# Performance work log

Hardware: AMD Instinct MI355X
Metric: run time of the kernel (lower is better)

The kernel has to match this reference:

```python
import jax, jax.numpy as jnp
import numpy as np
import math

H, DK, G_DIM, S_DIM, HID = 8, 64, 512, 3072, 512
B = 16384
EPS = 1e-5

def _layernorm(x, g, b):
    mu = jnp.mean(x, axis=-1, keepdims=True)
    var = jnp.mean((x - mu) ** 2, axis=-1, keepdims=True)
    return (x - mu) * jax.lax.rsqrt(var + EPS) * g + b

def setup_inputs() -> dict:
    key = jax.random.key(0)
    ks = jax.random.split(key, 12)
    s = 0.02
    return {
        "h_g": jax.random.normal(ks[0], (B, G_DIM), jnp.float32),
        "h_s": jax.random.normal(ks[1], (B, S_DIM), jnp.float32),
        # stacked per-head projections: [H, in_dim, d_k]
        "Wq": jax.random.normal(ks[2], (H, G_DIM, DK), jnp.float32) * s,
        "bq": jnp.zeros((H, DK), jnp.float32),
        "Wk": jax.random.normal(ks[3], (H, S_DIM, DK), jnp.float32) * s,
        "bk": jnp.zeros((H, DK), jnp.float32),
        "Wv": jax.random.normal(ks[4], (H, S_DIM, DK), jnp.float32) * s,
        "bv": jnp.zeros((H, DK), jnp.float32),
        "Wo": jax.random.normal(ks[5], (HID, HID), jnp.float32) * s,
        "bo": jnp.zeros((HID,), jnp.float32),
        "ln1_g": jnp.ones((HID,), jnp.float32),
        "ln1_b": jnp.zeros((HID,), jnp.float32),
        "W1": jax.random.normal(ks[6], (HID, 2 * HID), jnp.float32) * s,
        "b1": jnp.zeros((2 * HID,), jnp.float32),
        "W2": jax.random.normal(ks[7], (2 * HID, HID), jnp.float32) * s,
        "b2": jnp.zeros((HID,), jnp.float32),
        "ln2_g": jnp.ones((HID,), jnp.float32),
        "ln2_b": jnp.zeros((HID,), jnp.float32),
    }

def reference(h_g, h_s, Wq, bq, Wk, bk, Wv, bv, Wo, bo, ln1_g, ln1_b, W1, b1, W2, b2, ln2_g, ln2_b):
    b = h_g.shape[0]
    # batched per-head projections (fuses the per-head Linear loop)
    Q = jnp.einsum('bg,hgd->bhd', h_g, Wq) + bq          # [B,H,DK]
    K = jnp.einsum('bs,hsd->bhd', h_s, Wk) + bk          # [B,H,DK]
    V = jnp.einsum('bs,hsd->bhd', h_s, Wv) + bv          # [B,H,DK]
    # seq_len == 1: scores is [B,H,1]; softmax over a single key == 1
    scores = jnp.sum(Q * K, axis=-1, keepdims=True) / math.sqrt(DK)
    attn_w = jax.nn.softmax(scores, axis=-1)             # identically ones
    attn = attn_w * V                                    # == V
    h_concat = attn.reshape(b, H * DK)                   # [B,HID]
    h_attn = h_concat @ Wo + bo
    h_attn = _layernorm(h_attn + h_g, ln1_g, ln1_b)
    # MLP (dropout is identity in eval mode); torch GELU default = exact erf
    h = jax.nn.gelu(h_attn @ W1 + b1, approximate=False) @ W2 + b2
    return _layernorm(h + h_attn, ln2_g, ln2_b)
```

## Files before the change

kernel.cpp:

```cpp
#include <hip/hip_runtime.h>
#include <hip/hip_bf16.h>
#include <math.h>

#define HH    8
#define DKK   64
#define GD    512
#define SD    3072
#define HID_  512
#define BB    16384

typedef unsigned short ushort_t;
typedef __attribute__((ext_vector_type(8))) short bf16x8;
typedef __attribute__((ext_vector_type(4))) float f32x4;

__device__ __forceinline__ float bf2f(ushort_t u) {
  union { unsigned int i; float f; } c; c.i = ((unsigned int)u) << 16; return c.f;
}
__device__ __forceinline__ ushort_t f2bf(float f) {
  union { float f; unsigned int i; } c; c.f = f;
  unsigned int x = c.i;
  return (ushort_t)((x + 0x7FFFu + ((x >> 16) & 1u)) >> 16);
}
__device__ __forceinline__ unsigned int pk_bf16(float a, float b) {
  __hip_bfloat162 h = __float22bfloat162_rn(make_float2(a, b));
  union { __hip_bfloat162 h; unsigned int u; } c; c.h = h; return c.u;
}

__device__ __forceinline__ void async_cp16(const ushort_t* gsrc, ushort_t* ldst) {
  __builtin_amdgcn_global_load_lds(
      (const __attribute__((address_space(1))) unsigned int*)gsrc,
      (__attribute__((address_space(3))) unsigned int*)ldst, 16, 0, 0);
}
__device__ __forceinline__ void async_cp16f(const float* gsrc, float* ldst) {
  __builtin_amdgcn_global_load_lds(
      (const __attribute__((address_space(1))) unsigned int*)gsrc,
      (__attribute__((address_space(3))) unsigned int*)ldst, 16, 0, 0);
}

__device__ __forceinline__ float gelu_tanh(float x) {
  float y = 0.79788456080286535588f * (x + 0.044715f * x * x * x);
  float e = __expf(2.0f * y);
  float th = 1.0f - 2.0f / (e + 1.0f);
  return 0.5f * x * (1.0f + th);
}

__device__ __forceinline__ void swz_coords(int& nb, int& mb, int& kz) {
  int NB = gridDim.x, MB = gridDim.y;
  int bid = blockIdx.x + NB * (blockIdx.y + MB * blockIdx.z);
  int xcd = bid & 7;
  int j = bid >> 3;
  nb = j & (NB - 1);
  int rest = j / NB;
  int mk = (rest << 3) | xcd;
  mb = mk & (MB - 1);
  kz = mk / MB;
}

template <int EPI, int SWZ>
__global__ __launch_bounds__(256) void gemm_bt(
    const ushort_t* __restrict__ A, const ushort_t* __restrict__ Bt,
    void* __restrict__ Cv, const float* __restrict__ bias,
    int M, int N, int Kfull, int Klen) {
  __shared__ __align__(16) ushort_t As[128 * 32];
  __shared__ __align__(16) ushort_t Bs[128 * 32];
  const int tid = threadIdx.x;
  const int wv = tid >> 6;
  const int lane = tid & 63;
  int nb, mb, kz;
  if (SWZ) swz_coords(nb, mb, kz);
  else { nb = blockIdx.x; mb = blockIdx.y; kz = blockIdx.z; }
  const int m0 = mb * 128, n0 = nb * 128, kbeg = kz * Klen;
  const int srow = lane >> 2;
  const int scol = (lane & 3) * 8;
  const int wm = wv & 1, wn = wv >> 1;
  const int lr = lane & 15, quad = lane >> 4;

  f32x4 acc[4][4];
#pragma unroll
  for (int i = 0; i < 4; ++i)
#pragma unroll
    for (int j = 0; j < 4; ++j) acc[i][j] = (f32x4){0.f, 0.f, 0.f, 0.f};

  const ushort_t* Ab = A + (size_t)m0 * Kfull + kbeg;
  const ushort_t* Bb = Bt + (size_t)n0 * Kfull + kbeg;

  for (int k0 = 0; k0 < Klen; k0 += 32) {
    __syncthreads();
#pragma unroll
    for (int i = 0; i < 2; ++i) {
      const int chunk = i * 4 + wv;
      const int row = chunk * 16 + srow;
      async_cp16(Ab + (size_t)row * Kfull + (k0 + scol), As + chunk * 512);
      async_cp16(Bb + (size_t)row * Kfull + (k0 + scol), Bs + chunk * 512);
    }
    __syncthreads();
    bf16x8 af[4], bfr[4];
#pragma unroll
    for (int i = 0; i < 4; ++i)
      af[i] = *(const bf16x8*)&As[(wm * 64 + i * 16 + lr) * 32 + quad * 8];
#pragma unroll
    for (int j = 0; j < 4; ++j)
      bfr[j] = *(const bf16x8*)&Bs[(wn * 64 + j * 16 + lr) * 32 + quad * 8];
#pragma unroll
    for (int i = 0; i < 4; ++i)
#pragma unroll
      for (int j = 0; j < 4; ++j)
        acc[i][j] = __builtin_amdgcn_mfma_f32_16x16x32_bf16(af[i], bfr[j], acc[i][j], 0, 0, 0);
  }

#pragma unroll
  for (int i = 0; i < 4; ++i) {
    const int mg = m0 + wm * 64 + i * 16 + quad * 4;
#pragma unroll
    for (int j = 0; j < 4; ++j) {
      const int ng = n0 + wn * 64 + j * 16 + lr;
      if (EPI == 2) {
        float* C = (float*)Cv + (size_t)kz * M * N;
#pragma unroll
        for (int r = 0; r < 4; ++r)
          C[(size_t)(mg + r) * N + ng] = acc[i][j][r];
      } else {
        ushort_t* C = (ushort_t*)Cv;
        const float bvv = bias ? bias[ng] : 0.0f;
#pragma unroll
        for (int r = 0; r < 4; ++r) {
          float v = acc[i][j][r] + bvv;
          if (EPI == 1) v = gelu_tanh(v);
          C[(size_t)(mg + r) * N + ng] = f2bf(v);
        }
      }
    }
  }
}

__global__ __launch_bounds__(256, 4) void gemm_a32(
    const float* __restrict__ A, const ushort_t* __restrict__ Bt,
    float* __restrict__ C, int M, int N, int Kfull, int Klen) {
  __shared__ __align__(16) float As4[128 * 32];
  __shared__ __align__(16) ushort_t Bs[128 * 32];
  const int tid = threadIdx.x;
  const int wv = tid >> 6;
  const int lane = tid & 63;
  int nb, mb, kz;
  swz_coords(nb, mb, kz);
  const int m0 = mb * 128, n0 = nb * 128, kbeg = kz * Klen;
  const int srow = lane >> 2;
  const int scol = (lane & 3) * 8;
  const int wm = wv & 1, wn = wv >> 1;
  const int lr = lane & 15, quad = lane >> 4;
  const int a_rc = lane >> 3;
  const int a_g = (lane & 7) ^ a_rc;

  f32x4 acc[4][4];
#pragma unroll
  for (int i = 0; i < 4; ++i)
#pragma unroll
    for (int j = 0; j < 4; ++j) acc[i][j] = (f32x4){0.f, 0.f, 0.f, 0.f};

  const float* Ab = A + (size_t)m0 * Kfull + kbeg;
  const ushort_t* Bb = Bt + (size_t)n0 * Kfull + kbeg;

  for (int k0 = 0; k0 < Klen; k0 += 32) {
    __syncthreads();
#pragma unroll
    for (int i = 0; i < 2; ++i) {
      const int chunk = i * 4 + wv;
      const int row = chunk * 16 + srow;
      async_cp16(Bb + (size_t)row * Kfull + (k0 + scol), Bs + chunk * 512);
    }
#pragma unroll
    for (int t = 0; t < 4; ++t) {
      const int chunkA = t * 4 + wv;
      const int r = chunkA * 8 + a_rc;
      async_cp16f(Ab + (size_t)r * Kfull + (k0 + 4 * a_g), As4 + chunkA * 256);
    }
    __syncthreads();
    bf16x8 af[4], bfr[4];
#pragma unroll
    for (int i = 0; i < 4; ++i) {
      const int r = wm * 64 + i * 16 + lr;
      const int x0 = (2 * quad) ^ (lr & 7);
      const int x1 = (2 * quad + 1) ^ (lr & 7);
      float4 fa = *(const float4*)&As4[r * 32 + x0 * 4];
      float4 fb = *(const float4*)&As4[r * 32 + x1 * 4];
      union { unsigned int u[4]; bf16x8 v; } c;
      c.u[0] = pk_bf16(fa.x, fa.y); c.u[1] = pk_bf16(fa.z, fa.w);
      c.u[2] = pk_bf16(fb.x, fb.y); c.u[3] = pk_bf16(fb.z, fb.w);
      af[i] = c.v;
    }
#pragma unroll
    for (int j = 0; j < 4; ++j)
      bfr[j] = *(const bf16x8*)&Bs[(wn * 64 + j * 16 + lr) * 32 + quad * 8];
#pragma unroll
    for (int i = 0; i < 4; ++i)
#pragma unroll
      for (int j = 0; j < 4; ++j)
        acc[i][j] = __builtin_amdgcn_mfma_f32_16x16x32_bf16(af[i], bfr[j], acc[i][j], 0, 0, 0);
  }

  float* Cp = C + (size_t)kz * M * N;
#pragma unroll
  for (int i = 0; i < 4; ++i) {
    const int mg = m0 + wm * 64 + i * 16 + quad * 4;
#pragma unroll
    for (int j = 0; j < 4; ++j) {
      const int ng = n0 + wn * 64 + j * 16 + lr;
#pragma unroll
      for (int r = 0; r < 4; ++r)
        Cp[(size_t)(mg + r) * N + ng] = acc[i][j][r];
    }
  }
}

__global__ __launch_bounds__(256) void permute_wv(const float* __restrict__ Wv,
                                                  ushort_t* __restrict__ Wvp) {
  const int idx = (blockIdx.x * 256 + threadIdx.x) * 8;
  const int s = idx >> 9;
  const int c = idx & 511;
  const float* src = Wv + (size_t)(c >> 6) * (SD * DKK) + (size_t)s * DKK + (c & 63);
  float4 a = *(const float4*)src;
  float4 b = *(const float4*)(src + 4);
  unsigned int p[4];
  p[0] = pk_bf16(a.x, a.y); p[1] = pk_bf16(a.z, a.w);
  p[2] = pk_bf16(b.x, b.y); p[3] = pk_bf16(b.z, b.w);
  *(uint4*)(Wvp + idx) = *(const uint4*)p;
}

__global__ __launch_bounds__(256) void transpose3(
    const float* __restrict__ s0, ushort_t* __restrict__ d0,
    const float* __restrict__ s1, ushort_t* __restrict__ d1,
    const float* __restrict__ s2, ushort_t* __restrict__ d2) {
  __shared__ ushort_t tile[32][33];
  const int z = blockIdx.z;
  const float* src = (z == 0) ? s0 : (z == 1) ? s1 : s2;
  ushort_t* dst = (z == 0) ? d0 : (z == 1) ? d1 : d2;
  const int R = (z == 2) ? 1024 : 512;
  const int C = (z == 1) ? 1024 : 512;
  const int bx = blockIdx.x * 32;
  const int by = blockIdx.y * 32;
  if (bx >= C || by >= R) return;
  const int tx = threadIdx.x, ty = threadIdx.y;
#pragma unroll
  for (int i = 0; i < 32; i += 8)
    tile[ty + i][tx] = f2bf(src[(size_t)(by + ty + i) * C + (bx + tx)]);
  __syncthreads();
#pragma unroll
  for (int i = 0; i < 32; i += 8)
    dst[(size_t)(bx + ty + i) * R + (by + tx)] = tile[tx][ty + i];
}

__global__ __launch_bounds__(256) void c0_kernel(const float* __restrict__ bv,
                                                 const float* __restrict__ Wo,
                                                 const float* __restrict__ bo,
                                                 float* __restrict__ c0) {
  __shared__ float red[8][32];
  const int jl = threadIdx.x & 31;
  const int chunk = threadIdx.x >> 5;
  const int j = blockIdx.x * 32 + jl;
  const int cbase = chunk * 64;
  float s = 0.f;
#pragma unroll 8
  for (int c = 0; c < 64; ++c) s += bv[cbase + c] * Wo[(size_t)(cbase + c) * 512 + j];
  red[chunk][jl] = s;
  __syncthreads();
  if (chunk == 0) {
    float t = bo[j];
#pragma unroll
    for (int q = 0; q < 8; ++q) t += red[q][jl];
    c0[j] = t;
  }
}

template <int RES_F32, int OUT_F32>
__global__ __launch_bounds__(256) void ln_fused(const float* __restrict__ p0,
                                                const float* __restrict__ p1,
                                                const float* __restrict__ cb,
                                                const void* __restrict__ res_,
                                                const float* __restrict__ g,
                                                const float* __restrict__ b,
                                                void* __restrict__ out_) {
  const int row = blockIdx.x * 4 + (threadIdx.x >> 6);
  const int lane = threadIdx.x & 63;
  const size_t base = (size_t)row * 512 + lane * 8;
  const int col = lane * 8;
  float4 a0 = *(const float4*)(p0 + base);
  float4 a1 = *(const float4*)(p0 + base + 4);
  float4 c0v = *(const float4*)(p1 + base);
  float4 c1v = *(const float4*)(p1 + base + 4);
  float4 d0 = *(const float4*)(cb + col);
  float4 d1 = *(const float4*)(cb + col + 4);
  float t[8];
  t[0] = a0.x + c0v.x + d0.x; t[1] = a0.y + c0v.y + d0.y;
  t[2] = a0.z + c0v.z + d0.z; t[3] = a0.w + c0v.w + d0.w;
  t[4] = a1.x + c1v.x + d1.x; t[5] = a1.y + c1v.y + d1.y;
  t[6] = a1.z + c1v.z + d1.z; t[7] = a1.w + c1v.w + d1.w;
  float r[8];
  if (RES_F32) {
    const float* res = (const float*)res_;
    float4 e0 = *(const float4*)(res + base);
    float4 e1 = *(const float4*)(res + base + 4);
    r[0] = e0.x; r[1] = e0.y; r[2] = e0.z; r[3] = e0.w;
    r[4] = e1.x; r[5] = e1.y; r[6] = e1.z; r[7] = e1.w;
  } else {
    const ushort_t* res = (const ushort_t*)res_;
    uint4 rv = *(const uint4*)(res + base);
    const ushort_t* rp = (const ushort_t*)&rv;
#pragma unroll
    for (int k = 0; k < 8; ++k) r[k] = bf2f(rp[k]);
  }
  float x[8];
  float s = 0.f, sq = 0.f;
#pragma unroll
  for (int k = 0; k < 8; ++k) {
    float v = t[k] + r[k];
    x[k] = v; s += v; sq += v * v;
  }
#pragma unroll
  for (int off = 32; off > 0; off >>= 1) {
    s += __shfl_xor(s, off);
    sq += __shfl_xor(sq, off);
  }
  const float mean = s * (1.0f / 512.0f);
  const float var = sq * (1.0f / 512.0f) - mean * mean;
  const float rstd = rsqrtf(var + 1e-5f);
  float4 gv0 = *(const float4*)(g + col);
  float4 gv1 = *(const float4*)(g + col + 4);
  float4 bv0 = *(const float4*)(b + col);
  float4 bv1 = *(const float4*)(b + col + 4);
  const float gg[8] = {gv0.x, gv0.y, gv0.z, gv0.w, gv1.x, gv1.y, gv1.z, gv1.w};
  const float bb[8] = {bv0.x, bv0.y, bv0.z, bv0.w, bv1.x, bv1.y, bv1.z, bv1.w};
  float y[8];
#pragma unroll
  for (int k = 0; k < 8; ++k) y[k] = (x[k] - mean) * rstd * gg[k] + bb[k];
  if (OUT_F32) {
    float* out = (float*)out_;
    *(float4*)(out + base) = make_float4(y[0], y[1], y[2], y[3]);
    *(float4*)(out + base + 4) = make_float4(y[4], y[5], y[6], y[7]);
  } else {
    ushort_t* out = (ushort_t*)out_;
    uint4 ov; ushort_t* op = (ushort_t*)&ov;
#pragma unroll
    for (int k = 0; k < 8; ++k) op[k] = f2bf(y[k]);
    *(uint4*)(out + base) = ov;
  }
}

extern "C" void kernel_launch(void* const* d_in, const int* in_sizes, int n_in,
                              void* d_out, int out_size, void* d_ws, size_t ws_size,
                              hipStream_t stream) {
  const float* h_g  = (const float*)d_in[0];
  const float* h_s  = (const float*)d_in[1];
  const float* Wv   = (const float*)d_in[6];
  const float* bv   = (const float*)d_in[7];
  const float* Wo   = (const float*)d_in[8];
  const float* bo   = (const float*)d_in[9];
  const float* ln1g = (const float*)d_in[10];
  const float* ln1b = (const float*)d_in[11];
  const float* W1   = (const float*)d_in[12];
  const float* b1   = (const float*)d_in[13];
  const float* W2   = (const float*)d_in[14];
  const float* b2   = (const float*)d_in[15];
  const float* ln2g = (const float*)d_in[16];
  const float* ln2b = (const float*)d_in[17];

  char* ws = (char*)d_ws;
  ushort_t* WoT = (ushort_t*)(ws + 0);
  ushort_t* W1T = (ushort_t*)(ws + 524288);
  ushort_t* W2T = (ushort_t*)(ws + 1572864);
  ushort_t* Wvp = (ushort_t*)(ws + 2621440);
  ushort_t* WcT = (ushort_t*)(ws + 5767168);
  float*    c0f = (float*)(ws + 8912896);
  float*    p0  = (float*)(ws + 16777216);
  float*    p1  = (float*)(ws + 50331648);
  ushort_t* x   = (ushort_t*)(ws + 83886080);
  ushort_t* u   = (ushort_t*)(ws + 100663296);
  float*    q0  = p0;
  float*    q1  = p1;
  (void)in_sizes; (void)n_in; (void)out_size; (void)ws_size;

  hipLaunchKernelGGL(permute_wv, dim3(768), dim3(256), 0, stream, Wv, Wvp);
  hipLaunchKernelGGL(transpose3, dim3(32, 32, 3), dim3(32, 8), 0, stream,
                     Wo, WoT, W1, W1T, W2, W2T);
  hipLaunchKernelGGL(c0_kernel, dim3(16), dim3(256), 0, stream, bv, Wo, bo, c0f);

  hipLaunchKernelGGL((gemm_bt<0, 0>), dim3(24, 4, 1), dim3(256), 0, stream,
                     WoT, Wvp, (void*)WcT, (const float*)nullptr, 512, 3072, 512, 512);
  hipLaunchKernelGGL(gemm_a32, dim3(4, 128, 2), dim3(256), 0, stream,
                     h_s, WcT, p0, BB, 512, 3072, 1536);
  hipLaunchKernelGGL((ln_fused<1, 0>), dim3(4096), dim3(256), 0, stream,
                     p0, p1, c0f, (const void*)h_g, ln1g, ln1b, (void*)x);
  hipLaunchKernelGGL((gemm_bt<1, 1>), dim3(8, 128, 1), dim3(256), 0, stream,
                     x, W1T, (void*)u, b1, BB, 1024, 512, 512);
  hipLaunchKernelGGL((gemm_bt<2, 1>), dim3(4, 128, 2), dim3(256), 0, stream,
                     u, W2T, (void*)q0, (const float*)nullptr, BB, 512, 1024, 512);
  hipLaunchKernelGGL((ln_fused<0, 1>), dim3(4096), dim3(256), 0, stream,
                     q0, q1, b2, (const void*)x, ln2g, ln2b, d_out);
}
```

Baseline: 548.6 us.

## Double-buffer LDS tiles in both GEMM kernels to overlap loads with MFMA

Both GEMM kernels now keep two shared-memory buffers per operand. The next K-tile's async global-to-LDS copies are issued right after the barrier, so they run while the current tile feeds the MFMAs. This also cuts the main loop to one barrier per tile, hiding global-memory latency that was previously exposed on each iteration. In exchange, LDS per block doubles, which for gemm_a32 (48KB) may lower the number of resident blocks per CU below its launch bound.

```diff
diff --git a/kernel.cpp b/kernel.cpp
--- a/kernel.cpp
+++ b/kernel.cpp
@@ -61,8 +61,8 @@
     const ushort_t* __restrict__ A, const ushort_t* __restrict__ Bt,
     void* __restrict__ Cv, const float* __restrict__ bias,
     int M, int N, int Kfull, int Klen) {
-  __shared__ __align__(16) ushort_t As[128 * 32];
-  __shared__ __align__(16) ushort_t Bs[128 * 32];
+  __shared__ __align__(16) ushort_t As[2][128 * 32];
+  __shared__ __align__(16) ushort_t Bs[2][128 * 32];
   const int tid = threadIdx.x;
   const int wv = tid >> 6;
   const int lane = tid & 63;
@@ -84,23 +84,29 @@
   const ushort_t* Ab = A + (size_t)m0 * Kfull + kbeg;
   const ushort_t* Bb = Bt + (size_t)n0 * Kfull + kbeg;
 
-  for (int k0 = 0; k0 < Klen; k0 += 32) {
-    __syncthreads();
+  auto stage = [&](int k0, int b) {
 #pragma unroll
     for (int i = 0; i < 2; ++i) {
       const int chunk = i * 4 + wv;
       const int row = chunk * 16 + srow;
-      async_cp16(Ab + (size_t)row * Kfull + (k0 + scol), As + chunk * 512);
-      async_cp16(Bb + (size_t)row * Kfull + (k0 + scol), Bs + chunk * 512);
-    }
+      async_cp16(Ab + (size_t)row * Kfull + (k0 + scol), &As[b][chunk * 512]);
+      async_cp16(Bb + (size_t)row * Kfull + (k0 + scol), &Bs[b][chunk * 512]);
+    }
+  };
+
+  const int nt = Klen >> 5;
+  stage(0, 0);
+  int buf = 0;
+  for (int t = 0; t < nt; ++t, buf ^= 1) {
     __syncthreads();
+    if (t + 1 < nt) stage((t + 1) << 5, buf ^ 1);
     bf16x8 af[4], bfr[4];
 #pragma unroll
     for (int i = 0; i < 4; ++i)
-      af[i] = *(const bf16x8*)&As[(wm * 64 + i * 16 + lr) * 32 + quad * 8];
+      af[i] = *(const bf16x8*)&As[buf][(wm * 64 + i * 16 + lr) * 32 + quad * 8];
 #pragma unroll
     for (int j = 0; j < 4; ++j)
-      bfr[j] = *(const bf16x8*)&Bs[(wn * 64 + j * 16 + lr) * 32 + quad * 8];
+      bfr[j] = *(const bf16x8*)&Bs[buf][(wn * 64 + j * 16 + lr) * 32 + quad * 8];
 #pragma unroll
     for (int i = 0; i < 4; ++i)
 #pragma unroll
@@ -136,8 +142,8 @@
 __global__ __launch_bounds__(256, 4) void gemm_a32(
     const float* __restrict__ A, const ushort_t* __restrict__ Bt,
     float* __restrict__ C, int M, int N, int Kfull, int Klen) {
-  __shared__ __align__(16) float As4[128 * 32];
-  __shared__ __align__(16) ushort_t Bs[128 * 32];
+  __shared__ __align__(16) float As4[2][128 * 32];
+  __shared__ __align__(16) ushort_t Bs[2][128 * 32];
   const int tid = threadIdx.x;
   const int wv = tid >> 6;
   const int lane = tid & 63;
@@ -160,29 +166,35 @@
   const float* Ab = A + (size_t)m0 * Kfull + kbeg;
   const ushort_t* Bb = Bt + (size_t)n0 * Kfull + kbeg;
 
-  for (int k0 = 0; k0 < Klen; k0 += 32) {
-    __syncthreads();
+  auto stage = [&](int k0, int b) {
 #pragma unroll
     for (int i = 0; i < 2; ++i) {
       const int chunk = i * 4 + wv;
       const int row = chunk * 16 + srow;
-      async_cp16(Bb + (size_t)row * Kfull + (k0 + scol), Bs + chunk * 512);
-    }
-#pragma unroll
-    for (int t = 0; t < 4; ++t) {
-      const int chunkA = t * 4 + wv;
+      async_cp16(Bb + (size_t)row * Kfull + (k0 + scol), &Bs[b][chunk * 512]);
+    }
+#pragma unroll
+    for (int t4 = 0; t4 < 4; ++t4) {
+      const int chunkA = t4 * 4 + wv;
       const int r = chunkA * 8 + a_rc;
-      async_cp16f(Ab + (size_t)r * Kfull + (k0 + 4 * a_g), As4 + chunkA * 256);
-    }
+      async_cp16f(Ab + (size_t)r * Kfull + (k0 + 4 * a_g), &As4[b][chunkA * 256]);
+    }
+  };
+
+  const int nt = Klen >> 5;
+  stage(0, 0);
+  int buf = 0;
+  for (int t = 0; t < nt; ++t, buf ^= 1) {
     __syncthreads();
+    if (t + 1 < nt) stage((t + 1) << 5, buf ^ 1);
     bf16x8 af[4], bfr[4];
 #pragma unroll
     for (int i = 0; i < 4; ++i) {
       const int r = wm * 64 + i * 16 + lr;
       const int x0 = (2 * quad) ^ (lr & 7);
       const int x1 = (2 * quad + 1) ^ (lr & 7);
-      float4 fa = *(const float4*)&As4[r * 32 + x0 * 4];
-      float4 fb = *(const float4*)&As4[r * 32 + x1 * 4];
+      float4 fa = *(const float4*)&As4[buf][r * 32 + x0 * 4];
+      float4 fb = *(const float4*)&As4[buf][r * 32 + x1 * 4];
       union { unsigned int u[4]; bf16x8 v; } c;
       c.u[0] = pk_bf16(fa.x, fa.y); c.u[1] = pk_bf16(fa.z, fa.w);
       c.u[2] = pk_bf16(fb.x, fb.y); c.u[3] = pk_bf16(fb.z, fb.w);
@@ -190,7 +202,7 @@
     }
 #pragma unroll
     for (int j = 0; j < 4; ++j)
-      bfr[j] = *(const bf16x8*)&Bs[(wn * 64 + j * 16 + lr) * 32 + quad * 8];
+      bfr[j] = *(const bf16x8*)&Bs[buf][(wn * 64 + j * 16 + lr) * 32 + quad * 8];
 #pragma unroll
     for (int i = 0; i < 4; ++i)
 #pragma unroll
```

After: 549.4 us. No clear change (+0.1%).

## Double-buffer and swizzle LDS in GEMMs, shrink N tile to 64

Applied to the files above, without the earlier changes.

The bf16 GEMM kernel now double-buffers its LDS tiles, issuing the next K-slice copy before computing the current one, which needs only one barrier per iteration. Both GEMM kernels XOR-swizzle the LDS column slot to cut bank conflicts. They also move to a 64-wide N tile with higher occupancy hints and twice as many blocks. The intent is to overlap loads with MFMA work and raise occupancy. The cost is less reuse of the A tile per block, so A is re-read from global memory more often.

```diff
diff --git a/kernel.cpp b/kernel.cpp
--- a/kernel.cpp
+++ b/kernel.cpp
@@ -56,55 +56,68 @@
   kz = mk / MB;
 }
 
-template <int EPI, int SWZ>
-__global__ __launch_bounds__(256) void gemm_bt(
+template <int EPI, int SWZ, int BN>
+__global__ __launch_bounds__(256, (BN == 64) ? 6 : 2) void gemm_bt(
     const ushort_t* __restrict__ A, const ushort_t* __restrict__ Bt,
     void* __restrict__ Cv, const float* __restrict__ bias,
     int M, int N, int Kfull, int Klen) {
-  __shared__ __align__(16) ushort_t As[128 * 32];
-  __shared__ __align__(16) ushort_t Bs[128 * 32];
+  constexpr int NF = BN / 32;
+  __shared__ __align__(16) ushort_t As[2][128 * 32];
+  __shared__ __align__(16) ushort_t Bs[2][BN * 32];
   const int tid = threadIdx.x;
   const int wv = tid >> 6;
   const int lane = tid & 63;
   int nb, mb, kz;
   if (SWZ) swz_coords(nb, mb, kz);
   else { nb = blockIdx.x; mb = blockIdx.y; kz = blockIdx.z; }
-  const int m0 = mb * 128, n0 = nb * 128, kbeg = kz * Klen;
+  const int m0 = mb * 128, n0 = nb * BN, kbeg = kz * Klen;
   const int srow = lane >> 2;
-  const int scol = (lane & 3) * 8;
+  const int scolg = (((lane & 3) ^ ((lane >> 3) & 3))) * 8;
   const int wm = wv & 1, wn = wv >> 1;
   const int lr = lane & 15, quad = lane >> 4;
-
-  f32x4 acc[4][4];
+  const int slotx = (quad ^ ((lr >> 1) & 3)) * 8;
+
+  f32x4 acc[4][NF];
 #pragma unroll
   for (int i = 0; i < 4; ++i)
 #pragma unroll
-    for (int j = 0; j < 4; ++j) acc[i][j] = (f32x4){0.f, 0.f, 0.f, 0.f};
+    for (int j = 0; j < NF; ++j) acc[i][j] = (f32x4){0.f, 0.f, 0.f, 0.f};
 
   const ushort_t* Ab = A + (size_t)m0 * Kfull + kbeg;
   const ushort_t* Bb = Bt + (size_t)n0 * Kfull + kbeg;
 
-  for (int k0 = 0; k0 < Klen; k0 += 32) {
-    __syncthreads();
+  auto stage = [&](int k0, int b) {
 #pragma unroll
     for (int i = 0; i < 2; ++i) {
       const int chunk = i * 4 + wv;
       const int row = chunk * 16 + srow;
-      async_cp16(Ab + (size_t)row * Kfull + (k0 + scol), As + chunk * 512);
-      async_cp16(Bb + (size_t)row * Kfull + (k0 + scol), Bs + chunk * 512);
-    }
+      async_cp16(Ab + (size_t)row * Kfull + (k0 + scolg), &As[b][chunk * 512]);
+    }
+#pragma unroll
+    for (int i = 0; i < BN / 64; ++i) {
+      const int chunk = i * 4 + wv;
+      const int row = chunk * 16 + srow;
+      async_cp16(Bb + (size_t)row * Kfull + (k0 + scolg), &Bs[b][chunk * 512]);
+    }
+  };
+
+  const int nt = Klen >> 5;
+  stage(0, 0);
+  int buf = 0;
+  for (int t = 0; t < nt; ++t, buf ^= 1) {
     __syncthreads();
-    bf16x8 af[4], bfr[4];
+    if (t + 1 < nt) stage((t + 1) << 5, buf ^ 1);
+    bf16x8 af[4], bfr[NF];
 #pragma unroll
     for (int i = 0; i < 4; ++i)
-      af[i] = *(const bf16x8*)&As[(wm * 64 + i * 16 + lr) * 32 + quad * 8];
-#pragma unroll
-    for (int j = 0; j < 4; ++j)
-      bfr[j] = *(const bf16x8*)&Bs[(wn * 64 + j * 16 + lr) * 32 + quad * 8];
+      af[i] = *(const bf16x8*)&As[buf][(wm * 64 + i * 16 + lr) * 32 + slotx];
+#pragma unroll
+    for (int j = 0; j < NF; ++j)
+      bfr[j] = *(const bf16x8*)&Bs[buf][(wn * (NF * 16) + j * 16 + lr) * 32 + slotx];
 #pragma unroll
     for (int i = 0; i < 4; ++i)
 #pragma unroll
-      for (int j = 0; j < 4; ++j)
+      for (int j = 0; j < NF; ++j)
         acc[i][j] = __builtin_amdgcn_mfma_f32_16x16x32_bf16(af[i], bfr[j], acc[i][j], 0, 0, 0);
   }
 
@@ -112,8 +125,8 @@
   for (int i = 0; i < 4; ++i) {
     const int mg = m0 + wm * 64 + i * 16 + quad * 4;
 #pragma unroll
-    for (int j = 0; j < 4; ++j) {
-      const int ng = n0 + wn * 64 + j * 16 + lr;
+    for (int j = 0; j < NF; ++j) {
+      const int ng = n0 + wn * (NF * 16) + j * 16 + lr;
       if (EPI == 2) {
         float* C = (float*)Cv + (size_t)kz * M * N;
 #pragma unroll
@@ -133,49 +146,46 @@
   }
 }
 
-__global__ __launch_bounds__(256, 4) void gemm_a32(
+__global__ __launch_bounds__(256, 5) void gemm_a32(
     const float* __restrict__ A, const ushort_t* __restrict__ Bt,
     float* __restrict__ C, int M, int N, int Kfull, int Klen) {
   __shared__ __align__(16) float As4[128 * 32];
-  __shared__ __align__(16) ushort_t Bs[128 * 32];
+  __shared__ __align__(16) ushort_t Bs[64 * 32];
   const int tid = threadIdx.x;
   const int wv = tid >> 6;
   const int lane = tid & 63;
   int nb, mb, kz;
   swz_coords(nb, mb, kz);
-  const int m0 = mb * 128, n0 = nb * 128, kbeg = kz * Klen;
+  const int m0 = mb * 128, n0 = nb * 64, kbeg = kz * Klen;
   const int srow = lane >> 2;
-  const int scol = (lane & 3) * 8;
+  const int b_colg = (((lane & 3) ^ ((lane >> 3) & 3))) * 8;
   const int wm = wv & 1, wn = wv >> 1;
   const int lr = lane & 15, quad = lane >> 4;
+  const int slotx = (quad ^ ((lr >> 1) & 3)) * 8;
   const int a_rc = lane >> 3;
   const int a_g = (lane & 7) ^ a_rc;
 
-  f32x4 acc[4][4];
+  f32x4 acc[4][2];
 #pragma unroll
   for (int i = 0; i < 4; ++i)
 #pragma unroll
-    for (int j = 0; j < 4; ++j) acc[i][j] = (f32x4){0.f, 0.f, 0.f, 0.f};
+    for (int j = 0; j < 2; ++j) acc[i][j] = (f32x4){0.f, 0.f, 0.f, 0.f};
 
   const float* Ab = A + (size_t)m0 * Kfull + kbeg;
   const ushort_t* Bb = Bt + (size_t)n0 * Kfull + kbeg;
 
   for (int k0 = 0; k0 < Klen; k0 += 32) {
     __syncthreads();
-#pragma unroll
-    for (int i = 0; i < 2; ++i) {
-      const int chunk = i * 4 + wv;
-      const int row = chunk * 16 + srow;
-      async_cp16(Bb + (size_t)row * Kfull + (k0 + scol), Bs + chunk * 512);
-    }
-#pragma unroll
-    for (int t = 0; t < 4; ++t) {
-      const int chunkA = t * 4 + wv;
+    async_cp16(Bb + (size_t)(wv * 16 + srow) * Kfull + (k0 + b_colg),
+               Bs + wv * 512);
+#pragma unroll
+    for (int t4 = 0; t4 < 4; ++t4) {
+      const int chunkA = t4 * 4 + wv;
       const int r = chunkA * 8 + a_rc;
       async_cp16f(Ab + (size_t)r * Kfull + (k0 + 4 * a_g), As4 + chunkA * 256);
     }
     __syncthreads();
-    bf16x8 af[4], bfr[4];
+    bf16x8 af[4], bfr[2];
 #pragma unroll
     for (int i = 0; i < 4; ++i) {
       const int r = wm * 64 + i * 16 + lr;
@@ -189,12 +199,12 @@
       af[i] = c.v;
     }
 #pragma unroll
-    for (int j = 0; j < 4; ++j)
-      bfr[j] = *(const bf16x8*)&Bs[(wn * 64 + j * 16 + lr) * 32 + quad * 8];
+    for (int j = 0; j < 2; ++j)
+      bfr[j] = *(const bf16x8*)&Bs[(wn * 32 + j * 16 + lr) * 32 + slotx];
 #pragma unroll
     for (int i = 0; i < 4; ++i)
 #pragma unroll
-      for (int j = 0; j < 4; ++j)
+      for (int j = 0; j < 2; ++j)
         acc[i][j] = __builtin_amdgcn_mfma_f32_16x16x32_bf16(af[i], bfr[j], acc[i][j], 0, 0, 0);
   }
 
@@ -203,8 +213,8 @@
   for (int i = 0; i < 4; ++i) {
     const int mg = m0 + wm * 64 + i * 16 + quad * 4;
 #pragma unroll
-    for (int j = 0; j < 4; ++j) {
-      const int ng = n0 + wn * 64 + j * 16 + lr;
+    for (int j = 0; j < 2; ++j) {
+      const int ng = n0 + wn * 32 + j * 16 + lr;
 #pragma unroll
       for (int r = 0; r < 4; ++r)
         Cp[(size_t)(mg + r) * N + ng] = acc[i][j][r];
@@ -383,15 +393,15 @@
                      Wo, WoT, W1, W1T, W2, W2T);
   hipLaunchKernelGGL(c0_kernel, dim3(16), dim3(256), 0, stream, bv, Wo, bo, c0f);
 
-  hipLaunchKernelGGL((gemm_bt<0, 0>), dim3(24, 4, 1), dim3(256), 0, stream,
+  hipLaunchKernelGGL((gemm_bt<0, 0, 128>), dim3(24, 4, 1), dim3(256), 0, stream,
                      WoT, Wvp, (void*)WcT, (const float*)nullptr, 512, 3072, 512, 512);
-  hipLaunchKernelGGL(gemm_a32, dim3(4, 128, 2), dim3(256), 0, stream,
+  hipLaunchKernelGGL(gemm_a32, dim3(8, 128, 2), dim3(256), 0, stream,
                      h_s, WcT, p0, BB, 512, 3072, 1536);
   hipLaunchKernelGGL((ln_fused<1, 0>), dim3(4096), dim3(256), 0, stream,
                      p0, p1, c0f, (const void*)h_g, ln1g, ln1b, (void*)x);
-  hipLaunchKernelGGL((gemm_bt<1, 1>), dim3(8, 128, 1), dim3(256), 0, stream,
+  hipLaunchKernelGGL((gemm_bt<1, 1, 64>), dim3(16, 128, 1), dim3(256), 0, stream,
                      x, W1T, (void*)u, b1, BB, 1024, 512, 512);
-  hipLaunchKernelGGL((gemm_bt<2, 1>), dim3(4, 128, 2), dim3(256), 0, stream,
+  hipLaunchKernelGGL((gemm_bt<2, 1, 64>), dim3(8, 128, 2), dim3(256), 0, stream,
                      u, W2T, (void*)q0, (const float*)nullptr, BB, 512, 1024, 512);
   hipLaunchKernelGGL((ln_fused<0, 1>), dim3(4096), dim3(256), 0, stream,
                      q0, q1, b2, (const void*)x, ln2g, ln2b, d_out);
```

Result: slower. 578.4 us (+5.4%).

## Replace split-K fp32-A GEMM with 8-wave 128x256 double-buffered pipelined kernel

Applied to the files above, without the earlier changes.

The big h_s × WcT GEMM (K=3072) used a 128x128 tile, split-K over 2, and synchronous single-buffer staging. It now uses a 512-thread block computing a 128x256 tile over the full K. Tiles of 64 K-steps are double-buffered in 128KB of dynamic LDS, with async copies interleaved between MFMA phases, setprio, and XCD-aware block mapping. This removes the split-K partial buffer and lets the first LayerNorm read a single partial. The risk is lower occupancy and only 256 blocks, which may underfill the GPU.

```diff
diff --git a/kernel.cpp b/kernel.cpp
--- a/kernel.cpp
+++ b/kernel.cpp
@@ -133,23 +133,30 @@
   }
 }
 
-__global__ __launch_bounds__(256, 4) void gemm_a32(
+__global__ __launch_bounds__(512, 2) void gemm8_a32(
     const float* __restrict__ A, const ushort_t* __restrict__ Bt,
-    float* __restrict__ C, int M, int N, int Kfull, int Klen) {
-  __shared__ __align__(16) float As4[128 * 32];
-  __shared__ __align__(16) ushort_t Bs[128 * 32];
+    float* __restrict__ C, int M, int N, int K) {
+  extern __shared__ char smem[];
+  float* Af = (float*)smem;
+  ushort_t* Bsm = (ushort_t*)(smem + 65536);
   const int tid = threadIdx.x;
   const int wv = tid >> 6;
   const int lane = tid & 63;
-  int nb, mb, kz;
-  swz_coords(nb, mb, kz);
-  const int m0 = mb * 128, n0 = nb * 128, kbeg = kz * Klen;
-  const int srow = lane >> 2;
-  const int scol = (lane & 3) * 8;
-  const int wm = wv & 1, wn = wv >> 1;
   const int lr = lane & 15, quad = lane >> 4;
-  const int a_rc = lane >> 3;
-  const int a_g = (lane & 7) ^ a_rc;
+  const int wm = wv >> 2, wn = wv & 3;
+  const int bid = blockIdx.x + (int)gridDim.x * blockIdx.y;
+  const int xcd = bid & 7;
+  const int jj = bid >> 3;
+  const int nb = jj & 1;
+  const int mb = xcd * 16 + (jj >> 1);
+  const int m0 = mb * 128, n0 = nb * 256;
+
+  const int a_r0 = wv * 4 + (lane >> 4);
+  const int a_g = (lane & 15) ^ ((wv & 1) * 4 + (lane >> 4));
+  const float* Asrc = A + (size_t)(m0 + a_r0) * K + a_g * 4;
+  const int b_r0 = wv * 8 + (lane >> 3);
+  const int b_g = (lane & 7) ^ (lane >> 3);
+  const ushort_t* Bsrc = Bt + (size_t)(n0 + b_r0) * K + b_g * 8;
 
   f32x4 acc[4][4];
 #pragma unroll
@@ -157,57 +164,158 @@
 #pragma unroll
     for (int j = 0; j < 4; ++j) acc[i][j] = (f32x4){0.f, 0.f, 0.f, 0.f};
 
-  const float* Ab = A + (size_t)m0 * Kfull + kbeg;
-  const ushort_t* Bb = Bt + (size_t)n0 * Kfull + kbeg;
-
-  for (int k0 = 0; k0 < Klen; k0 += 32) {
-    __syncthreads();
+  auto stageA2 = [&](int k0, int b, int i0) {
 #pragma unroll
     for (int i = 0; i < 2; ++i) {
-      const int chunk = i * 4 + wv;
-      const int row = chunk * 16 + srow;
-      async_cp16(Bb + (size_t)row * Kfull + (k0 + scol), Bs + chunk * 512);
-    }
-#pragma unroll
-    for (int t = 0; t < 4; ++t) {
-      const int chunkA = t * 4 + wv;
-      const int r = chunkA * 8 + a_rc;
-      async_cp16f(Ab + (size_t)r * Kfull + (k0 + 4 * a_g), As4 + chunkA * 256);
-    }
-    __syncthreads();
-    bf16x8 af[4], bfr[4];
-#pragma unroll
-    for (int i = 0; i < 4; ++i) {
-      const int r = wm * 64 + i * 16 + lr;
-      const int x0 = (2 * quad) ^ (lr & 7);
-      const int x1 = (2 * quad + 1) ^ (lr & 7);
-      float4 fa = *(const float4*)&As4[r * 32 + x0 * 4];
-      float4 fb = *(const float4*)&As4[r * 32 + x1 * 4];
-      union { unsigned int u[4]; bf16x8 v; } c;
-      c.u[0] = pk_bf16(fa.x, fa.y); c.u[1] = pk_bf16(fa.z, fa.w);
-      c.u[2] = pk_bf16(fb.x, fb.y); c.u[3] = pk_bf16(fb.z, fb.w);
-      af[i] = c.v;
-    }
-#pragma unroll
-    for (int j = 0; j < 4; ++j)
-      bfr[j] = *(const bf16x8*)&Bs[(wn * 64 + j * 16 + lr) * 32 + quad * 8];
-#pragma unroll
-    for (int i = 0; i < 4; ++i)
-#pragma unroll
-      for (int j = 0; j < 4; ++j)
-        acc[i][j] = __builtin_amdgcn_mfma_f32_16x16x32_bf16(af[i], bfr[j], acc[i][j], 0, 0, 0);
-  }
-
-  float* Cp = C + (size_t)kz * M * N;
-#pragma unroll
-  for (int i = 0; i < 4; ++i) {
-    const int mg = m0 + wm * 64 + i * 16 + quad * 4;
-#pragma unroll
-    for (int j = 0; j < 4; ++j) {
-      const int ng = n0 + wn * 64 + j * 16 + lr;
+      const int ii = i0 + i;
+      async_cp16f(Asrc + (size_t)(ii * 32) * K + k0,
+                  Af + b * 8192 + ii * 2048 + wv * 256);
+    }
+  };
+  auto stageB2 = [&](int k0, int b, int i0) {
+#pragma unroll
+    for (int i = 0; i < 2; ++i) {
+      const int ii = i0 + i;
+      async_cp16(Bsrc + (size_t)(ii * 64) * K + k0,
+                 Bsm + b * 16384 + ii * 4096 + wv * 512);
+    }
+  };
+
+  stageA2(0, 0, 0); stageA2(0, 0, 2);
+  stageB2(0, 0, 0); stageB2(0, 0, 2);
+  stageA2(64, 1, 0); stageA2(64, 1, 2);
+  asm volatile("s_waitcnt vmcnt(4)" ::: "memory");
+  __builtin_amdgcn_sched_barrier(0);
+  __builtin_amdgcn_s_barrier();
+
+  const int nt = K >> 6;
+  for (int t = 0; t < nt; ++t) {
+    const int b = t & 1;
+    const int kB = (t + 1) << 6;
+    const int kA = (t + 2) << 6;
+    const bool hasB = (t + 1 < nt);
+    const bool hasA = (t + 2 < nt);
+    const float* Ab = Af + b * 8192;
+    const ushort_t* Bb = Bsm + b * 16384;
+
+    bf16x8 bfr[4][2];
+#pragma unroll
+    for (int jf = 0; jf < 4; ++jf) {
+      const int r = wn * 64 + jf * 16 + lr;
+#pragma unroll
+      for (int kk = 0; kk < 2; ++kk) {
+        const int pg = (kk * 4 + quad) ^ (lr & 7);
+        bfr[jf][kk] = *(const bf16x8*)(Bb + r * 64 + pg * 8);
+      }
+    }
+    bf16x8 af0[2], af1[2], af2[2], af3[2];
+    {
+      const float* base0 = Ab + (wm * 64 + 0 * 16 + lr) * 64;
+      const float* base1 = Ab + (wm * 64 + 1 * 16 + lr) * 64;
+#pragma unroll
+      for (int kk = 0; kk < 2; ++kk) {
+        const int g0 = (kk * 8 + 2 * quad) ^ (lr & 7);
+        const int g1 = (kk * 8 + 2 * quad + 1) ^ (lr & 7);
+        float4 fa = *(const float4*)(base0 + g0 * 4);
+        float4 fb = *(const float4*)(base0 + g1 * 4);
+        union { unsigned int u[4]; bf16x8 v; } c0;
+        c0.u[0] = pk_bf16(fa.x, fa.y); c0.u[1] = pk_bf16(fa.z, fa.w);
+        c0.u[2] = pk_bf16(fb.x, fb.y); c0.u[3] = pk_bf16(fb.z, fb.w);
+        af0[kk] = c0.v;
+        float4 ga = *(const float4*)(base1 + g0 * 4);
+        float4 gb = *(const float4*)(base1 + g1 * 4);
+        union { unsigned int u[4]; bf16x8 v; } c1;
+        c1.u[0] = pk_bf16(ga.x, ga.y); c1.u[1] = pk_bf16(ga.z, ga.w);
+        c1.u[2] = pk_bf16(gb.x, gb.y); c1.u[3] = pk_bf16(gb.z, gb.w);
+        af1[kk] = c1.v;
+      }
+    }
+    if (hasB) stageB2(kB, b ^ 1, 0);
+    __builtin_amdgcn_s_barrier();
+    __builtin_amdgcn_s_setprio(1);
+#pragma unroll
+    for (int jf = 0; jf < 4; ++jf) {
+      acc[0][jf] = __builtin_amdgcn_mfma_f32_16x16x32_bf16(af0[0], bfr[jf][0], acc[0][jf], 0, 0, 0);
+      acc[0][jf] = __builtin_amdgcn_mfma_f32_16x16x32_bf16(af0[1], bfr[jf][1], acc[0][jf], 0, 0, 0);
+    }
+    __builtin_amdgcn_s_setprio(0);
+    asm volatile("s_waitcnt lgkmcnt(0)" ::: "memory");
+    __builtin_amdgcn_sched_barrier(0);
+    __builtin_amdgcn_s_barrier();
+
+    {
+      const float* base2 = Ab + (wm * 64 + 2 * 16 + lr) * 64;
+      const float* base3 = Ab + (wm * 64 + 3 * 16 + lr) * 64;
+#pragma unroll
+      for (int kk = 0; kk < 2; ++kk) {
+        const int g0 = (kk * 8 + 2 * quad) ^ (lr & 7);
+        const int g1 = (kk * 8 + 2 * quad + 1) ^ (lr & 7);
+        float4 fa = *(const float4*)(base2 + g0 * 4);
+        float4 fb = *(const float4*)(base2 + g1 * 4);
+        union { unsigned int u[4]; bf16x8 v; } c2;
+        c2.u[0] = pk_bf16(fa.x, fa.y); c2.u[1] = pk_bf16(fa.z, fa.w);
+        c2.u[2] = pk_bf16(fb.x, fb.y); c2.u[3] = pk_bf16(fb.z, fb.w);
+        af2[kk] = c2.v;
+        float4 ga = *(const float4*)(base3 + g0 * 4);
+        float4 gb = *(const float4*)(base3 + g1 * 4);
+        union { unsigned int u[4]; bf16x8 v; } c3;
+        c3.u[0] = pk_bf16(ga.x, ga.y); c3.u[1] = pk_bf16(ga.z, ga.w);
+        c3.u[2] = pk_bf16(gb.x, gb.y); c3.u[3] = pk_bf16(gb.z, gb.w);
+        af3[kk] = c3.v;
+      }
+    }
+    if (hasB) stageB2(kB, b ^ 1, 2);
+    __builtin_amdgcn_s_barrier();
+    __builtin_amdgcn_s_setprio(1);
+#pragma unroll
+    for (int jf = 0; jf < 4; ++jf) {
+      acc[1][jf] = __builtin_amdgcn_mfma_f32_16x16x32_bf16(af1[0], bfr[jf][0], acc[1][jf], 0, 0, 0);
+      acc[1][jf] = __builtin_amdgcn_mfma_f32_16x16x32_bf16(af1[1], bfr[jf][1], acc[1][jf], 0, 0, 0);
+    }
+    __builtin_amdgcn_s_setprio(0);
+    asm volatile("s_waitcnt lgkmcnt(0)" ::: "memory");
+    __builtin_amdgcn_sched_barrier(0);
+    __builtin_amdgcn_s_barrier();
+
+    if (hasA) stageA2(kA, b, 0);
+    __builtin_amdgcn_s_barrier();
+    __builtin_amdgcn_s_setprio(1);
+#pragma unroll
+    for (int jf = 0; jf < 4; ++jf) {
+      acc[2][jf] = __builtin_amdgcn_mfma_f32_16x16x32_bf16(af2[0], bfr[jf][0], acc[2][jf], 0, 0, 0);
+      acc[2][jf] = __builtin_amdgcn_mfma_f32_16x16x32_bf16(af2[1], bfr[jf][1], acc[2][jf], 0, 0, 0);
+    }
+    __builtin_amdgcn_s_setprio(0);
+    __builtin_amdgcn_sched_barrier(0);
+    __builtin_amdgcn_s_barrier();
+
+    if (hasA) stageA2(kA, b, 2);
+    __builtin_amdgcn_s_barrier();
+    __builtin_amdgcn_s_setprio(1);
+#pragma unroll
+    for (int jf = 0; jf < 4; ++jf) {
+      acc[3][jf] = __builtin_amdgcn_mfma_f32_16x16x32_bf16(af3[0], bfr[jf][0], acc[3][jf], 0, 0, 0);
+      acc[3][jf] = __builtin_amdgcn_mfma_f32_16x16x32_bf16(af3[1], bfr[jf][1], acc[3][jf], 0, 0, 0);
+    }
+    __builtin_amdgcn_s_setprio(0);
+    if (t < nt - 2) {
+      asm volatile("s_waitcnt vmcnt(4)" ::: "memory");
+    } else {
+      asm volatile("s_waitcnt vmcnt(0)" ::: "memory");
+    }
+    __builtin_amdgcn_sched_barrier(0);
+    __builtin_amdgcn_s_barrier();
+  }
+
+#pragma unroll
+  for (int m = 0; m < 4; ++m) {
+    const int mg = m0 + wm * 64 + m * 16 + quad * 4;
+#pragma unroll
+    for (int jf = 0; jf < 4; ++jf) {
+      const int ng = n0 + wn * 64 + jf * 16 + lr;
 #pragma unroll
       for (int r = 0; r < 4; ++r)
-        Cp[(size_t)(mg + r) * N + ng] = acc[i][j][r];
+        C[(size_t)(mg + r) * N + ng] = acc[m][jf][r];
     }
   }
 }
@@ -271,7 +379,7 @@
   }
 }
 
-template <int RES_F32, int OUT_F32>
+template <int RES_F32, int OUT_F32, int TWO_P>
 __global__ __launch_bounds__(256) void ln_fused(const float* __restrict__ p0,
                                                 const float* __restrict__ p1,
                                                 const float* __restrict__ cb,
@@ -285,15 +393,19 @@
   const int col = lane * 8;
   float4 a0 = *(const float4*)(p0 + base);
   float4 a1 = *(const float4*)(p0 + base + 4);
-  float4 c0v = *(const float4*)(p1 + base);
-  float4 c1v = *(const float4*)(p1 + base + 4);
   float4 d0 = *(const float4*)(cb + col);
   float4 d1 = *(const float4*)(cb + col + 4);
   float t[8];
-  t[0] = a0.x + c0v.x + d0.x; t[1] = a0.y + c0v.y + d0.y;
-  t[2] = a0.z + c0v.z + d0.z; t[3] = a0.w + c0v.w + d0.w;
-  t[4] = a1.x + c1v.x + d1.x; t[5] = a1.y + c1v.y + d1.y;
-  t[6] = a1.z + c1v.z + d1.z; t[7] = a1.w + c1v.w + d1.w;
+  t[0] = a0.x + d0.x; t[1] = a0.y + d0.y;
+  t[2] = a0.z + d0.z; t[3] = a0.w + d0.w;
+  t[4] = a1.x + d1.x; t[5] = a1.y + d1.y;
+  t[6] = a1.z + d1.z; t[7] = a1.w + d1.w;
+  if (TWO_P) {
+    float4 c0v = *(const float4*)(p1 + base);
+    float4 c1v = *(const float4*)(p1 + base + 4);
+    t[0] += c0v.x; t[1] += c0v.y; t[2] += c0v.z; t[3] += c0v.w;
+    t[4] += c1v.x; t[5] += c1v.y; t[6] += c1v.z; t[7] += c1v.w;
+  }
   float r[8];
   if (RES_F32) {
     const float* res = (const float*)res_;
@@ -385,14 +497,15 @@
 
   hipLaunchKernelGGL((gemm_bt<0, 0>), dim3(24, 4, 1), dim3(256), 0, stream,
                      WoT, Wvp, (void*)WcT, (const float*)nullptr, 512, 3072, 512, 512);
-  hipLaunchKernelGGL(gemm_a32, dim3(4, 128, 2), dim3(256), 0, stream,
-                     h_s, WcT, p0, BB, 512, 3072, 1536);
-  hipLaunchKernelGGL((ln_fused<1, 0>), dim3(4096), dim3(256), 0, stream,
-                     p0, p1, c0f, (const void*)h_g, ln1g, ln1b, (void*)x);
+  hipLaunchKernelGGL(gemm8_a32, dim3(2, 128, 1), dim3(512), 131072, stream,
+                     h_s, WcT, p0, BB, 512, 3072);
+  hipLaunchKernelGGL((ln_fused<1, 0, 0>), dim3(4096), dim3(256), 0, stream,
+                     p0, (const float*)nullptr, c0f, (const void*)h_g,
+                     ln1g, ln1b, (void*)x);
   hipLaunchKernelGGL((gemm_bt<1, 1>), dim3(8, 128, 1), dim3(256), 0, stream,
                      x, W1T, (void*)u, b1, BB, 1024, 512, 512);
   hipLaunchKernelGGL((gemm_bt<2, 1>), dim3(4, 128, 2), dim3(256), 0, stream,
                      u, W2T, (void*)q0, (const float*)nullptr, BB, 512, 1024, 512);
-  hipLaunchKernelGGL((ln_fused<0, 1>), dim3(4096), dim3(256), 0, stream,
+  hipLaunchKernelGGL((ln_fused<0, 1, 1>), dim3(4096), dim3(256), 0, stream,
                      q0, q1, b2, (const void*)x, ln2g, ln2b, d_out);
 }
```

After: 505.0 us. -8.0%, faster.
